# Kernel tuning notes

Hardware: AMD Instinct MI355X
Metric: run time of the kernel (lower is better)

Reference implementation:

```python
import jax, jax.numpy as jnp
import numpy as np

BETA_MEM = 0.9
BETA_INH = 0.6
THRESHOLD = 1.0  # snn.Leaky default


def setup_inputs() -> dict:
    key = jax.random.key(0)
    k1, = jax.random.split(key, 1)
    T, B = 1024, 16384
    spike_seq = (jax.random.uniform(k1, (T, B, 2)) < 0.05).astype(jnp.float32)
    w_exc = jnp.array([[0.7, 1.0]], dtype=jnp.float32)  # fc_exc.weight, [1, 2]
    w_inh = jnp.array(-1.0, dtype=jnp.float32)          # scalar inhibitory weight
    return {"spike_seq": spike_seq, "w_exc": w_exc, "w_inh": w_inh}


@jax.custom_vjp
def spike_fn(x):
    # Heaviside spike with ATan surrogate gradient (snntorch default, alpha=2)
    return (x > 0).astype(x.dtype)

def _spike_fwd(x):
    return spike_fn(x), x

def _spike_bwd(x, g):
    return (g / (1.0 + (jnp.pi * x) ** 2),)

spike_fn.defvjp(_spike_fwd, _spike_bwd)


def reference(spike_seq, w_exc, w_inh):
    T, B, _ = spike_seq.shape
    mem0 = jnp.zeros((B, 1), dtype=spike_seq.dtype)
    inh0 = jnp.zeros((B, 1), dtype=spike_seq.dtype)

    def step(carry, x_t):
        mem, inh = carry
        cur_exc = x_t @ w_exc.T                      # [B, 1]
        fm1 = x_t[:, 0:1]                            # [B, 1]
        inh = BETA_INH * inh + fm1
        cur = cur_exc + w_inh * inh
        # snn.Leaky: reset (subtract) computed from previous mem, detached
        reset = jax.lax.stop_gradient((mem - THRESHOLD > 0).astype(mem.dtype))
        mem = BETA_MEM * mem + cur - reset * THRESHOLD
        spk = spike_fn(mem - THRESHOLD)
        return (mem, inh), (spk, mem)

    _, (spk_rec, mem_rec) = jax.lax.scan(step, (mem0, inh0), spike_seq)
    return spk_rec, mem_rec  # each [T, B, 1]
```

## Files before the change

### kernel.cpp

```cpp
#include <hip/hip_runtime.h>

#define T_LEN 1024
#define B_N   16384
#define NSEG  8
#define SEGT  (T_LEN / NSEG)
#define GN    256
#define PH2   8
#define NPH2  (SEGT / PH2)
#define CW_WORDS (B_N * (T_LEN / 16))

__global__ __launch_bounds__(256) void k1_compress(
    const float* __restrict__ x, unsigned int* __restrict__ cw) {
  const int tid = blockIdx.x * 256 + threadIdx.x;
  const int pn  = tid & (B_N / 2 - 1);
  const int j   = tid >> 13;
  const float4* xp4 = (const float4*)x;
  unsigned int wA = 0, wB = 0;
#pragma unroll
  for (int k = 0; k < 16; ++k) {
    const float4 v = xp4[(size_t)(16 * j + k) * (B_N / 2) + pn];
    wA |= (v.x != 0.0f ? 1u : 0u) << (2 * k);
    wA |= (v.y != 0.0f ? 1u : 0u) << (2 * k + 1);
    wB |= (v.z != 0.0f ? 1u : 0u) << (2 * k);
    wB |= (v.w != 0.0f ? 1u : 0u) << (2 * k + 1);
  }
  ((uint2*)cw)[(size_t)j * (B_N / 2) + pn] = make_uint2(wA, wB);
}

__global__ __launch_bounds__(64, 1) void k2a_checkpoint(
    const unsigned int* __restrict__ cw,
    const float* __restrict__ w_exc, const float* __restrict__ w_inh,
    float2* __restrict__ chk) {
#pragma clang fp contract(off)
  const int n = blockIdx.x * 64 + threadIdx.x;
  const float w0 = w_exc[0], w1 = w_exc[1], wi = w_inh[0];
  float mem = 0.0f, inh = 0.0f;
  unsigned int A = cw[n];
  unsigned int Bw = cw[(size_t)1 * B_N + n];
  unsigned int C = cw[(size_t)2 * B_N + n];
  unsigned int D = cw[(size_t)3 * B_N + n];

#define STEP16(W)                                                   \
  _Pragma("unroll") for (int k = 0; k < 16; ++k) {                  \
    const float x0 = (float)(((W) >> (2 * k)) & 1u);                \
    const float x1 = (float)(((W) >> (2 * k + 1)) & 1u);            \
    const float cur_exc = x0 * w0 + x1 * w1;   \
    inh = 0.6f * inh + x0;                                          \
    const float cur = cur_exc + wi * inh;          \
    const float reset = (mem > 1.0f) ? 1.0f : 0.0f;                 \
    mem = 0.9f * mem + cur - reset;           \
  }

  for (int j = 0; j < 56; j += 4) {
    unsigned int nA = 0, nB = 0, nC = 0, nD = 0;
    if (j + 4 < 56) {
      nA = cw[(size_t)(j + 4) * B_N + n];
      nB = cw[(size_t)(j + 5) * B_N + n];
      nC = cw[(size_t)(j + 6) * B_N + n];
      nD = cw[(size_t)(j + 7) * B_N + n];
    }
    __builtin_amdgcn_sched_barrier(0);
    STEP16(A) STEP16(Bw) STEP16(C) STEP16(D)
    if (((j + 4) & 7) == 0)
      chk[(size_t)(((j + 4) >> 3) - 1) * B_N + n] = make_float2(mem, inh);
    A = nA; Bw = nB; C = nC; D = nD;
  }
#undef STEP16
}

__shared__ __align__(16) float SPK[2][PH2][GN];
__shared__ __align__(16) float MEM[2][PH2][GN];

static __device__ __forceinline__ void block_barrier() {
  asm volatile("" ::: "memory");
  __builtin_amdgcn_s_barrier();
  asm volatile("" ::: "memory");
}

__global__ __launch_bounds__(384, 1) void FMFMNeuronInhib_34033320854098_kernel(
    const unsigned int* __restrict__ cw, const float2* __restrict__ chk,
    const float* __restrict__ w_exc, const float* __restrict__ w_inh,
    float* __restrict__ out) {
#pragma clang fp contract(off)
  const int lane = threadIdx.x & 63;
  const int wid  = threadIdx.x >> 6;
  const int seg  = blockIdx.x >> 6;
  const int g    = blockIdx.x & 63;
  const int nb0  = g * GN;
  const int tseg = seg * SEGT;

  if (wid < 4) {
    const int nloc = wid * 64 + lane;
    const int n    = nb0 + nloc;
    const float w0 = w_exc[0], w1 = w_exc[1], wi = w_inh[0];
    float mem = 0.0f, inh = 0.0f;
    if (seg > 0) {
      const float2 c = chk[(size_t)(seg - 1) * B_N + n];
      mem = c.x; inh = c.y;
    }
    unsigned int wcur = cw[(size_t)(seg * 8) * B_N + n];
    for (int jl = 0; jl < 8; ++jl) {
      unsigned int wnext = 0u;
      if (jl < 7) wnext = cw[(size_t)(seg * 8 + jl + 1) * B_N + n];
#pragma unroll
      for (int half = 0; half < 2; ++half) {
#pragma unroll
        for (int u = 0; u < 8; ++u) {
          const int k = half * 8 + u;
          const float x0 = (float)((wcur >> (2 * k)) & 1u);
          const float x1 = (float)((wcur >> (2 * k + 1)) & 1u);
          const float cur_exc = x0 * w0 + x1 * w1;
          inh = 0.6f * inh + x0;
          const float cur = cur_exc + wi * inh;
          const float reset = (mem > 1.0f) ? 1.0f : 0.0f;
          mem = 0.9f * mem + cur - reset;
          const float spk = (mem > 1.0f) ? 1.0f : 0.0f;
          SPK[half][u][nloc] = spk;
          MEM[half][u][nloc] = mem;
        }
        asm volatile("s_waitcnt lgkmcnt(0)" ::: "memory");
        block_barrier();
      }
      wcur = wnext;
    }
  } else {
    float* gout = (wid == 4) ? out : out + (size_t)T_LEN * B_N;
    const float* plane = (wid == 4) ? &SPK[0][0][0] : &MEM[0][0][0];
    const int n0 = lane * 4;
    auto drain = [&](int p) {
      const int slot = p & 1;
      const int t0   = tseg + p * PH2;
#pragma unroll
      for (int r = 0; r < PH2; ++r) {
        const float4 v =
            *(const float4*)(plane + ((size_t)slot * PH2 + r) * GN + n0);
        *(float4*)&gout[(size_t)(t0 + r) * B_N + nb0 + n0] = v;
      }
      asm volatile("s_waitcnt lgkmcnt(0)" ::: "memory");
    };
    for (int p = 0; p < NPH2; ++p) {
      if (p >= 1) drain(p - 1);
      block_barrier();
    }
    drain(NPH2 - 1);
  }
}

extern "C" void kernel_launch(void* const* d_in, const int* in_sizes, int n_in,
                              void* d_out, int out_size, void* d_ws, size_t ws_size,
                              hipStream_t stream) {
  const float* x     = (const float*)d_in[0];
  const float* w_exc = (const float*)d_in[1];
  const float* w_inh = (const float*)d_in[2];
  float* out = (float*)d_out;
  unsigned int* cw = (unsigned int*)d_ws;
  float2* chk = (float2*)((char*)d_ws + (size_t)CW_WORDS * 4);

  hipLaunchKernelGGL(k1_compress, dim3(CW_WORDS / 2 / 256), dim3(256), 0,
                     stream, x, cw);
  hipLaunchKernelGGL(k2a_checkpoint, dim3(B_N / 64), dim3(64), 0, stream,
                     cw, w_exc, w_inh, chk);
  hipLaunchKernelGGL(FMFMNeuronInhib_34033320854098_kernel,
                     dim3(NSEG * (B_N / GN)), dim3(384), 0, stream,
                     cw, chk, w_exc, w_inh, out);
}
```

Before: 270.9 us.

## Drop LDS producer/consumer staging; compute waves store outputs directly

Removes the warp-specialized scheme in which four compute waves wrote spikes and membrane values into a double-buffered LDS and two drain waves copied them to global memory as float4 rows. Each of 256 threads now preloads all 8 compressed words for its segment, runs the recurrence fully unrolled, and writes scalar coalesced stores straight to global memory. A block barrier after every 16 steps keeps the waves roughly in step. This removes the LDS traffic and the producer/consumer synchronisation and allows two blocks per CU, but gives up wide stores and the separate drain waves that overlapped stores with compute.

```diff
diff --git a/kernel.cpp b/kernel.cpp
--- a/kernel.cpp
+++ b/kernel.cpp
@@ -5,8 +5,6 @@
 #define NSEG  8
 #define SEGT  (T_LEN / NSEG)
 #define GN    256
-#define PH2   8
-#define NPH2  (SEGT / PH2)
 #define CW_WORDS (B_N * (T_LEN / 16))
 
 __global__ __launch_bounds__(256) void k1_compress(
@@ -68,81 +66,47 @@
 #undef STEP16
 }
 
-__shared__ __align__(16) float SPK[2][PH2][GN];
-__shared__ __align__(16) float MEM[2][PH2][GN];
-
-static __device__ __forceinline__ void block_barrier() {
-  asm volatile("" ::: "memory");
-  __builtin_amdgcn_s_barrier();
-  asm volatile("" ::: "memory");
-}
-
-__global__ __launch_bounds__(384, 1) void FMFMNeuronInhib_34033320854098_kernel(
+__global__ __launch_bounds__(256, 2) void FMFMNeuronInhib_34033320854098_kernel(
     const unsigned int* __restrict__ cw, const float2* __restrict__ chk,
     const float* __restrict__ w_exc, const float* __restrict__ w_inh,
     float* __restrict__ out) {
 #pragma clang fp contract(off)
-  const int lane = threadIdx.x & 63;
-  const int wid  = threadIdx.x >> 6;
-  const int seg  = blockIdx.x >> 6;
-  const int g    = blockIdx.x & 63;
-  const int nb0  = g * GN;
-  const int tseg = seg * SEGT;
+  const int seg = blockIdx.x >> 6;
+  const int g   = blockIdx.x & 63;
+  const int n   = g * GN + threadIdx.x;
 
-  if (wid < 4) {
-    const int nloc = wid * 64 + lane;
-    const int n    = nb0 + nloc;
-    const float w0 = w_exc[0], w1 = w_exc[1], wi = w_inh[0];
-    float mem = 0.0f, inh = 0.0f;
-    if (seg > 0) {
-      const float2 c = chk[(size_t)(seg - 1) * B_N + n];
-      mem = c.x; inh = c.y;
+  float* __restrict__ spk_out = out;
+  float* __restrict__ mem_out = out + (size_t)T_LEN * B_N;
+
+  const float w0 = w_exc[0], w1 = w_exc[1], wi = w_inh[0];
+  float mem = 0.0f, inh = 0.0f;
+  if (seg > 0) {
+    const float2 c = chk[(size_t)(seg - 1) * B_N + n];
+    mem = c.x;
+    inh = c.y;
+  }
+  unsigned int w[8];
+#pragma unroll
+  for (int j = 0; j < 8; ++j) w[j] = cw[(size_t)(seg * 8 + j) * B_N + n];
+
+#pragma unroll
+  for (int j = 0; j < 8; ++j) {
+#pragma unroll
+    for (int k = 0; k < 16; ++k) {
+      const int t = seg * SEGT + j * 16 + k;
+      const float x0 = (float)((w[j] >> (2 * k)) & 1u);
+      const float x1 = (float)((w[j] >> (2 * k + 1)) & 1u);
+      const float cur_exc = x0 * w0 + x1 * w1;
+      inh = 0.6f * inh + x0;
+      const float cur = cur_exc + wi * inh;
+      const float reset = (mem > 1.0f) ? 1.0f : 0.0f;
+      mem = 0.9f * mem + cur - reset;
+      const float spk = (mem > 1.0f) ? 1.0f : 0.0f;
+      const size_t idx = (size_t)t * B_N + n;
+      spk_out[idx] = spk;
+      mem_out[idx] = mem;
     }
-    unsigned int wcur = cw[(size_t)(seg * 8) * B_N + n];
-    for (int jl = 0; jl < 8; ++jl) {
-      unsigned int wnext = 0u;
-      if (jl < 7) wnext = cw[(size_t)(seg * 8 + jl + 1) * B_N + n];
-#pragma unroll
-      for (int half = 0; half < 2; ++half) {
-#pragma unroll
-        for (int u = 0; u < 8; ++u) {
-          const int k = half * 8 + u;
-          const float x0 = (float)((wcur >> (2 * k)) & 1u);
-          const float x1 = (float)((wcur >> (2 * k + 1)) & 1u);
-          const float cur_exc = x0 * w0 + x1 * w1;
-          inh = 0.6f * inh + x0;
-          const float cur = cur_exc + wi * inh;
-          const float reset = (mem > 1.0f) ? 1.0f : 0.0f;
-          mem = 0.9f * mem + cur - reset;
-          const float spk = (mem > 1.0f) ? 1.0f : 0.0f;
-          SPK[half][u][nloc] = spk;
-          MEM[half][u][nloc] = mem;
-        }
-        asm volatile("s_waitcnt lgkmcnt(0)" ::: "memory");
-        block_barrier();
-      }
-      wcur = wnext;
-    }
-  } else {
-    float* gout = (wid == 4) ? out : out + (size_t)T_LEN * B_N;
-    const float* plane = (wid == 4) ? &SPK[0][0][0] : &MEM[0][0][0];
-    const int n0 = lane * 4;
-    auto drain = [&](int p) {
-      const int slot = p & 1;
-      const int t0   = tseg + p * PH2;
-#pragma unroll
-      for (int r = 0; r < PH2; ++r) {
-        const float4 v =
-            *(const float4*)(plane + ((size_t)slot * PH2 + r) * GN + n0);
-        *(float4*)&gout[(size_t)(t0 + r) * B_N + nb0 + n0] = v;
-      }
-      asm volatile("s_waitcnt lgkmcnt(0)" ::: "memory");
-    };
-    for (int p = 0; p < NPH2; ++p) {
-      if (p >= 1) drain(p - 1);
-      block_barrier();
-    }
-    drain(NPH2 - 1);
+    __builtin_amdgcn_s_barrier();
   }
 }
 
@@ -161,6 +125,6 @@
   hipLaunchKernelGGL(k2a_checkpoint, dim3(B_N / 64), dim3(64), 0, stream,
                      cw, w_exc, w_inh, chk);
   hipLaunchKernelGGL(FMFMNeuronInhib_34033320854098_kernel,
-                     dim3(NSEG * (B_N / GN)), dim3(384), 0, stream,
+                     dim3(NSEG * (B_N / GN)), dim3(GN), 0, stream,
                      cw, chk, w_exc, w_inh, out);
 }
```

Measured after the change: 270.3 us. Within noise of the previous version (-0.2%).
